# Optimization experiments

Measured on AMD Instinct MI355X. Metric: run time of the kernel, lower is better.

The kernel has to match this reference:

```python
import jax, jax.numpy as jnp
import numpy as np

B, T, D = 2, 2048, 1024
H, DK = 16, 64          # num_heads, head_dim (expand_v=1 -> d_v == d_k)
K = 4                    # short conv kernel size
EPS = 1e-5               # gated RMSNorm eps


def setup_inputs() -> dict:
    key = jax.random.key(0)
    ks = jax.random.split(key, 12)
    s = lambda d: d ** -0.5
    return {
        "x": jax.random.normal(ks[0], (B, T, D), jnp.float32),
        "Wq": jax.random.normal(ks[1], (D, H * DK), jnp.float32) * s(D),
        "Wk": jax.random.normal(ks[2], (D, H * DK), jnp.float32) * s(D),
        "Wv": jax.random.normal(ks[3], (D, H * DK), jnp.float32) * s(D),
        "Wa": jax.random.normal(ks[4], (D, H), jnp.float32) * s(D),
        "Wb": jax.random.normal(ks[5], (D, H), jnp.float32) * s(D),
        "Wg": jax.random.normal(ks[6], (D, H * DK), jnp.float32) * s(D),
        "Wo": jax.random.normal(ks[7], (H * DK, D), jnp.float32) * s(H * DK),
        "conv_q": jax.random.normal(ks[8], (H * DK, K), jnp.float32) * s(K),
        "conv_k": jax.random.normal(ks[9], (H * DK, K), jnp.float32) * s(K),
        "conv_v": jax.random.normal(ks[10], (H * DK, K), jnp.float32) * s(K),
        "A_log": jnp.log(jax.random.uniform(ks[11], (H,), jnp.float32, 1.0, 16.0)),
        "dt_bias": jnp.full((H,), 0.5, jnp.float32),
        "rms_w": jnp.ones((DK,), jnp.float32),
    }


def _short_conv(x, w):
    # causal depthwise conv1d (no bias) + silu; x: [B,T,C], w: [C,K]
    kk = w.shape[1]
    xp = jnp.pad(x, ((0, 0), (kk - 1, 0), (0, 0))).transpose(0, 2, 1)  # [B,C,T+K-1]
    y = jax.lax.conv_general_dilated(xp, w[:, None, :], (1,), 'VALID',
                                     feature_group_count=w.shape[0])
    return jax.nn.silu(y.transpose(0, 2, 1))


def _l2norm(x):
    return x * jax.lax.rsqrt(jnp.sum(x * x, -1, keepdims=True) + 1e-6)


def _gated_delta_rule(q, k, v, g, beta):
    # q,k,v: [B,T,H,Dk], g,beta: [B,T,H]; gated delta-rule linear attention
    scale = q.shape[-1] ** -0.5
    q = _l2norm(q) * scale
    k = _l2norm(k)
    qs, ks_, vs, gs, bs = (jnp.moveaxis(a, 1, 0) for a in (q, k, v, g, beta))
    h0 = jnp.zeros((q.shape[0], q.shape[2], q.shape[3], v.shape[3]), q.dtype)

    def step(h, t):
        qt, kt, vt, gt, bt = t
        h = h * jnp.exp(gt)[..., None, None]                      # decay state
        v_adj = (vt - jnp.einsum('bhk,bhkv->bhv', kt, h)) * bt[..., None]
        h = h + kt[..., None] * v_adj[:, :, None, :]              # rank-1 delta update
        ot = jnp.einsum('bhk,bhkv->bhv', qt, h)
        return h, ot

    _, o = jax.lax.scan(step, h0, (qs, ks_, vs, gs, bs))
    return jnp.moveaxis(o, 0, 1)  # [B,T,H,Dv]


def reference(x, Wq, Wk, Wv, Wa, Wb, Wg, Wo, conv_q, conv_k, conv_v, A_log, dt_bias, rms_w):
    q = _short_conv(x @ Wq, conv_q).reshape(B, T, H, DK)
    k = _short_conv(x @ Wk, conv_k).reshape(B, T, H, DK)
    v = _short_conv(x @ Wv, conv_v).reshape(B, T, H, DK)
    g = -jnp.exp(A_log) * jax.nn.softplus(x @ Wa + dt_bias)   # [B,T,H] log-decay
    beta = jax.nn.sigmoid(x @ Wb)                             # [B,T,H]
    o = _gated_delta_rule(q, k, v, g, beta)                   # [B,T,H,DK]
    gate = (x @ Wg).reshape(B, T, H, DK)
    o = o * jax.lax.rsqrt(jnp.mean(o * o, -1, keepdims=True) + EPS) * rms_w
    o = o * jax.nn.silu(gate)                                 # gated RMSNorm
    return o.reshape(B, T, H * DK) @ Wo
```

## Files before the change

### kernel.cpp

```cpp
#include <hip/hip_runtime.h>
#include <hip/hip_bf16.h>
#include <math.h>
#include <stdint.h>

#define BB 2
#define TT 2048
#define DD 1024
#define HH 16
#define DK 64
#define HD 1024
#define NC 32
#define CL 64
#define PAD 68
#define VS 16

typedef short bf16x8 __attribute__((ext_vector_type(8)));
typedef float f32x4 __attribute__((ext_vector_type(4)));
typedef unsigned short u16x8 __attribute__((ext_vector_type(8)));
typedef unsigned short u16x4 __attribute__((ext_vector_type(4)));

#define GAS __attribute__((address_space(1)))
#define LAS __attribute__((address_space(3)))

#define DOT4(a, b) ((a).x*(b).x + (a).y*(b).y + (a).z*(b).z + (a).w*(b).w)

#define OUT16(acc, kf, wv) \
    acc[0][0] += kf.x * wv.x; acc[0][1] += kf.x * wv.y; acc[0][2] += kf.x * wv.z; acc[0][3] += kf.x * wv.w; \
    acc[1][0] += kf.y * wv.x; acc[1][1] += kf.y * wv.y; acc[1][2] += kf.y * wv.z; acc[1][3] += kf.y * wv.w; \
    acc[2][0] += kf.z * wv.x; acc[2][1] += kf.z * wv.y; acc[2][2] += kf.z * wv.z; acc[2][3] += kf.z * wv.w; \
    acc[3][0] += kf.w * wv.x; acc[3][1] += kf.w * wv.y; acc[3][2] += kf.w * wv.z; acc[3][3] += kf.w * wv.w;

#define WSUB(c, hv) \
    acc[0][0] -= wa0.c * hv.x; acc[0][1] -= wa0.c * hv.y; acc[0][2] -= wa0.c * hv.z; acc[0][3] -= wa0.c * hv.w; \
    acc[1][0] -= wa1.c * hv.x; acc[1][1] -= wa1.c * hv.y; acc[1][2] -= wa1.c * hv.z; acc[1][3] -= wa1.c * hv.w; \
    acc[2][0] -= wa2.c * hv.x; acc[2][1] -= wa2.c * hv.y; acc[2][2] -= wa2.c * hv.z; acc[2][3] -= wa2.c * hv.w; \
    acc[3][0] -= wa3.c * hv.x; acc[3][1] -= wa3.c * hv.y; acc[3][2] -= wa3.c * hv.z; acc[3][3] -= wa3.c * hv.w;

#define ACC16(c, wv) \
    acc[0][0] += sa0.c * wv.x; acc[0][1] += sa0.c * wv.y; acc[0][2] += sa0.c * wv.z; acc[0][3] += sa0.c * wv.w; \
    acc[1][0] += sa1.c * wv.x; acc[1][1] += sa1.c * wv.y; acc[1][2] += sa1.c * wv.z; acc[1][3] += sa1.c * wv.w; \
    acc[2][0] += sa2.c * wv.x; acc[2][1] += sa2.c * wv.y; acc[2][2] += sa2.c * wv.z; acc[2][3] += sa2.c * wv.w; \
    acc[3][0] += sa3.c * wv.x; acc[3][1] += sa3.c * wv.y; acc[3][2] += sa3.c * wv.z; acc[3][3] += sa3.c * wv.w;

__device__ __forceinline__ float sigmoidf_(float x) { return 1.0f / (1.0f + expf(-x)); }
__device__ __forceinline__ float siluf_(float x) { return x * sigmoidf_(x); }

__device__ __forceinline__ unsigned short f2bf(float f) {
    unsigned int u = __builtin_bit_cast(unsigned int, f);
    u = (u + 0x7fffu + ((u >> 16) & 1u)) >> 16;
    return (unsigned short)u;
}

__global__ __launch_bounds__(256) void castx_k(const float* __restrict__ src,
                                               unsigned short* __restrict__ dst) {
    const size_t idx = (size_t)blockIdx.x * 256 + threadIdx.x;
    float4 a = *(const float4*)&src[idx * 8];
    float4 b = *(const float4*)&src[idx * 8 + 4];
    u16x8 o;
    o[0] = f2bf(a.x); o[1] = f2bf(a.y); o[2] = f2bf(a.z); o[3] = f2bf(a.w);
    o[4] = f2bf(b.x); o[5] = f2bf(b.y); o[6] = f2bf(b.z); o[7] = f2bf(b.w);
    *(u16x8*)&dst[idx * 8] = o;
}

__global__ __launch_bounds__(256) void castw_k(const float* __restrict__ W,
                                               unsigned short* __restrict__ Wt) {
    __shared__ float t_s[64][65];
    const int tid = threadIdx.x;
    const int rr = tid >> 4;
    const int cc = tid & 15;
    const int r0 = blockIdx.y * 64;
    const int c0 = blockIdx.x * 64;
#pragma unroll
    for (int i = 0; i < 4; ++i) {
        const int row = rr + i * 16;
        float4 v = *(const float4*)&W[(size_t)(r0 + row) * 1024 + c0 + cc * 4];
        t_s[row][cc * 4 + 0] = v.x;
        t_s[row][cc * 4 + 1] = v.y;
        t_s[row][cc * 4 + 2] = v.z;
        t_s[row][cc * 4 + 3] = v.w;
    }
    __syncthreads();
#pragma unroll
    for (int i = 0; i < 4; ++i) {
        const int nr = rr + i * 16;
        u16x4 o;
#pragma unroll
        for (int d = 0; d < 4; ++d) o[d] = f2bf(t_s[cc * 4 + d][nr]);
        *(u16x4*)&Wt[(size_t)(c0 + nr) * 1024 + r0 + cc * 4] = o;
    }
}

__global__ __launch_bounds__(256) void tw_k(const float* __restrict__ Wa,
                                            const float* __restrict__ Wb,
                                            float* __restrict__ Wt) {
    const int o = blockIdx.x;
    const int h = o & 15;
    const float* W = (o < 16) ? Wa : Wb;
    const int tid = threadIdx.x;
    float4 v;
    v.x = W[(size_t)(tid * 4 + 0) * HH + h];
    v.y = W[(size_t)(tid * 4 + 1) * HH + h];
    v.z = W[(size_t)(tid * 4 + 2) * HH + h];
    v.w = W[(size_t)(tid * 4 + 3) * HH + h];
    *(float4*)&Wt[(size_t)o * DD + tid * 4] = v;
}

__global__ __launch_bounds__(256) void gemm_bf16_k(const unsigned short* __restrict__ A,
                                                   const unsigned short* __restrict__ Bt,
                                                   float* __restrict__ C,
                                                   int M, int N, int Kd) {
    __shared__ unsigned short a_s[128 * 32];
    __shared__ unsigned short b_s[128 * 32];

    const int tid = threadIdx.x;
    const int wave = tid >> 6;
    const int lane = tid & 63;
    const int m0 = blockIdx.y * 128;
    const int n0 = blockIdx.x * 128;

    const int quad = lane >> 4;
    const int l16 = lane & 15;
    const int wr = wave >> 1;
    const int wc = wave & 1;

    const int srow = lane >> 2;
    const int sseg = lane & 3;

    f32x4 acc[4][4];
#pragma unroll
    for (int i = 0; i < 4; ++i)
#pragma unroll
        for (int j = 0; j < 4; ++j) acc[i][j] = (f32x4){0.f, 0.f, 0.f, 0.f};

    for (int k0 = 0; k0 < Kd; k0 += 32) {
        __syncthreads();
#pragma unroll
        for (int c = 0; c < 2; ++c) {
            const int region = wave * 2 + c;
            const int r0t = region * 16;
            const int ra = r0t + srow;
            const unsigned short* ga = A + (size_t)(m0 + ra) * Kd + k0 + sseg * 8;
            const unsigned short* gb = Bt + (size_t)(n0 + ra) * Kd + k0 + sseg * 8;
            __builtin_amdgcn_global_load_lds((const GAS unsigned int*)ga,
                                             (LAS unsigned int*)&a_s[r0t * 32], 16, 0, 0);
            __builtin_amdgcn_global_load_lds((const GAS unsigned int*)gb,
                                             (LAS unsigned int*)&b_s[r0t * 32], 16, 0, 0);
        }
        __syncthreads();

        bf16x8 af[4], bfr[4];
#pragma unroll
        for (int i = 0; i < 4; ++i)
            af[i] = *(const bf16x8*)&a_s[(wr * 64 + i * 16 + l16) * 32 + quad * 8];
#pragma unroll
        for (int j = 0; j < 4; ++j)
            bfr[j] = *(const bf16x8*)&b_s[(wc * 64 + j * 16 + l16) * 32 + quad * 8];
#pragma unroll
        for (int i = 0; i < 4; ++i)
#pragma unroll
            for (int j = 0; j < 4; ++j)
                acc[i][j] = __builtin_amdgcn_mfma_f32_16x16x32_bf16(af[i], bfr[j], acc[i][j], 0, 0, 0);
    }

#pragma unroll
    for (int i = 0; i < 4; ++i)
#pragma unroll
        for (int j = 0; j < 4; ++j) {
            const int col = n0 + wc * 64 + j * 16 + l16;
#pragma unroll
            for (int r = 0; r < 4; ++r) {
                const int row = m0 + wr * 64 + i * 16 + quad * 4 + r;
                C[(size_t)row * N + col] = acc[i][j][r];
            }
        }
}

__global__ __launch_bounds__(256) void gemm_qkvg_k(const unsigned short* __restrict__ A,
                                                   const unsigned short* __restrict__ Bt,
                                                   float* __restrict__ Oq,
                                                   float* __restrict__ Ok,
                                                   float* __restrict__ Ov,
                                                   float* __restrict__ Og) {
    __shared__ unsigned short a_s[128 * 32];
    __shared__ unsigned short b_s[128 * 32];

    const int tid = threadIdx.x;
    const int wave = tid >> 6;
    const int lane = tid & 63;
    const int m0 = blockIdx.y * 128;
    const int n0 = blockIdx.x * 128;

    const int quad = lane >> 4;
    const int l16 = lane & 15;
    const int wr = wave >> 1;
    const int wc = wave & 1;

    const int srow = lane >> 2;
    const int sseg = lane & 3;

    f32x4 acc[4][4];
#pragma unroll
    for (int i = 0; i < 4; ++i)
#pragma unroll
        for (int j = 0; j < 4; ++j) acc[i][j] = (f32x4){0.f, 0.f, 0.f, 0.f};

    for (int k0 = 0; k0 < DD; k0 += 32) {
        __syncthreads();
#pragma unroll
        for (int c = 0; c < 2; ++c) {
            const int region = wave * 2 + c;
            const int r0t = region * 16;
            const int ra = r0t + srow;
            const unsigned short* ga = A + (size_t)(m0 + ra) * DD + k0 + sseg * 8;
            const unsigned short* gb = Bt + (size_t)(n0 + ra) * DD + k0 + sseg * 8;
            __builtin_amdgcn_global_load_lds((const GAS unsigned int*)ga,
                                             (LAS unsigned int*)&a_s[r0t * 32], 16, 0, 0);
            __builtin_amdgcn_global_load_lds((const GAS unsigned int*)gb,
                                             (LAS unsigned int*)&b_s[r0t * 32], 16, 0, 0);
        }
        __syncthreads();

        bf16x8 af[4], bfr[4];
#pragma unroll
        for (int i = 0; i < 4; ++i)
            af[i] = *(const bf16x8*)&a_s[(wr * 64 + i * 16 + l16) * 32 + quad * 8];
#pragma unroll
        for (int j = 0; j < 4; ++j)
            bfr[j] = *(const bf16x8*)&b_s[(wc * 64 + j * 16 + l16) * 32 + quad * 8];
#pragma unroll
        for (int i = 0; i < 4; ++i)
#pragma unroll
            for (int j = 0; j < 4; ++j)
                acc[i][j] = __builtin_amdgcn_mfma_f32_16x16x32_bf16(af[i], bfr[j], acc[i][j], 0, 0, 0);
    }

    float* Cd = (n0 < 1024) ? Oq : (n0 < 2048) ? Ok : (n0 < 3072) ? Ov : Og;
    const int nl = n0 & 1023;
#pragma unroll
    for (int i = 0; i < 4; ++i)
#pragma unroll
        for (int j = 0; j < 4; ++j) {
            const int col = nl + wc * 64 + j * 16 + l16;
#pragma unroll
            for (int r = 0; r < 4; ++r) {
                const int row = m0 + wr * 64 + i * 16 + quad * 4 + r;
                Cd[(size_t)row * HD + col] = acc[i][j][r];
            }
        }
}

__global__ __launch_bounds__(256) void gbeta_k(const float* __restrict__ x,
                                               const float* __restrict__ Wt,
                                               const float* __restrict__ A_log,
                                               const float* __restrict__ dt_bias,
                                               float* __restrict__ g,
                                               float* __restrict__ beta) {
    __shared__ __align__(16) float xs[8][DD];
    const int r0 = blockIdx.x * 8;
    const int tid = threadIdx.x;

#pragma unroll
    for (int i = 0; i < 8; ++i) {
        const int f = tid + i * 256;
        const int r = f >> 8;
        const int col = (f & 255) * 4;
        *(float4*)&xs[r][col] = *(const float4*)&x[((size_t)r0 + r) * DD + col];
    }
    __syncthreads();

    const int out = tid >> 3;
    const int part = tid & 7;
    const int h = out & 15;
    const float* Wrow = Wt + (size_t)out * DD;

    float a0 = 0, a1 = 0, a2 = 0, a3 = 0, a4 = 0, a5 = 0, a6 = 0, a7 = 0;
#pragma unroll 4
    for (int i = 0; i < 32; ++i) {
        const int d = i * 32 + part * 4;
        const float4 wv = *(const float4*)&Wrow[d];
        float4 x0 = *(const float4*)&xs[0][d];
        float4 x1 = *(const float4*)&xs[1][d];
        float4 x2 = *(const float4*)&xs[2][d];
        float4 x3 = *(const float4*)&xs[3][d];
        float4 x4 = *(const float4*)&xs[4][d];
        float4 x5 = *(const float4*)&xs[5][d];
        float4 x6 = *(const float4*)&xs[6][d];
        float4 x7 = *(const float4*)&xs[7][d];
        a0 += DOT4(x0, wv); a1 += DOT4(x1, wv);
        a2 += DOT4(x2, wv); a3 += DOT4(x3, wv);
        a4 += DOT4(x4, wv); a5 += DOT4(x5, wv);
        a6 += DOT4(x6, wv); a7 += DOT4(x7, wv);
    }
#pragma unroll
    for (int s = 1; s <= 4; s <<= 1) {
        a0 += __shfl_xor(a0, s); a1 += __shfl_xor(a1, s);
        a2 += __shfl_xor(a2, s); a3 += __shfl_xor(a3, s);
        a4 += __shfl_xor(a4, s); a5 += __shfl_xor(a5, s);
        a6 += __shfl_xor(a6, s); a7 += __shfl_xor(a7, s);
    }

    if (part == 0) {
        float sv[8] = {a0, a1, a2, a3, a4, a5, a6, a7};
        if (out < 16) {
            const float ae = -expf(A_log[h]);
            const float db = dt_bias[h];
#pragma unroll
            for (int r = 0; r < 8; ++r) {
                float v = sv[r] + db;
                float sp = (v > 20.0f) ? v : log1pf(expf(v));
                g[((size_t)r0 + r) * HH + h] = ae * sp;
            }
        } else {
#pragma unroll
            for (int r = 0; r < 8; ++r)
                beta[((size_t)r0 + r) * HH + h] = sigmoidf_(sv[r]);
        }
    }
}

__global__ __launch_bounds__(64) void stage_k(const float* __restrict__ q_pre,
                                              const float* __restrict__ k_pre,
                                              const float* __restrict__ cq,
                                              const float* __restrict__ ck,
                                              const float* __restrict__ g,
                                              float* __restrict__ Qc,
                                              float* __restrict__ Kc,
                                              float* __restrict__ bcum) {
    const int blk = blockIdx.x;
    const int bh = blk >> 5;
    const int c = blk & 31;
    const int b = bh >> 4;
    const int h = bh & 15;
    const int lane = threadIdx.x;
    const int ch = h * DK + lane;

    const float4 wq4 = *(const float4*)&cq[ch * 4];
    const float4 wk4 = *(const float4*)&ck[ch * 4];

    float qw0 = 0, qw1 = 0, qw2 = 0, kw0 = 0, kw1 = 0, kw2 = 0;
    {
        const int t0 = c * CL;
        if (t0 - 3 >= 0) { size_t bi = ((size_t)b * TT + t0 - 3) * HD + ch; qw0 = q_pre[bi]; kw0 = k_pre[bi]; }
        if (t0 - 2 >= 0) { size_t bi = ((size_t)b * TT + t0 - 2) * HD + ch; qw1 = q_pre[bi]; kw1 = k_pre[bi]; }
        if (t0 - 1 >= 0) { size_t bi = ((size_t)b * TT + t0 - 1) * HD + ch; qw2 = q_pre[bi]; kw2 = k_pre[bi]; }
    }
    float* Qo = Qc + (size_t)blk * 4096;
    float* Ko = Kc + (size_t)blk * 4096;

    for (int tt = 0; tt < CL; ++tt) {
        const int t = c * CL + tt;
        const size_t bi = ((size_t)b * TT + t) * HD + ch;
        const float qc_ = q_pre[bi];
        const float kc_ = k_pre[bi];
        float qa = qw0 * wq4.x + qw1 * wq4.y + qw2 * wq4.z + qc_ * wq4.w;
        float ka = kw0 * wk4.x + kw1 * wk4.y + kw2 * wk4.z + kc_ * wk4.w;
        qw0 = qw1; qw1 = qw2; qw2 = qc_;
        kw0 = kw1; kw1 = kw2; kw2 = kc_;
        qa = siluf_(qa);
        ka = siluf_(ka);
        float qs2 = qa * qa, ks2 = ka * ka;
#pragma unroll
        for (int s = 32; s > 0; s >>= 1) {
            qs2 += __shfl_xor(qs2, s);
            ks2 += __shfl_xor(ks2, s);
        }
        Qo[tt * 64 + lane] = qa * rsqrtf(qs2 + 1e-6f) * 0.125f;
        Ko[tt * 64 + lane] = ka * rsqrtf(ks2 + 1e-6f);
    }

    float cum = g[((size_t)b * TT + c * CL + lane) * HH + h];
#pragma unroll
    for (int s = 1; s < 64; s <<= 1) {
        float u = __shfl_up(cum, s);
        if (lane >= s) cum += u;
    }
    bcum[(size_t)blk * 64 + lane] = cum;
}

__global__ __launch_bounds__(256) void prep_k(const float* __restrict__ Kc,
                                              const float* __restrict__ v_pre,
                                              const float* __restrict__ cv,
                                              const float* __restrict__ bcum,
                                              const float* __restrict__ bbuf,
                                              float* __restrict__ Wv,
                                              float* __restrict__ Wk) {
    __shared__ __align__(16) float k_s[CL * PAD];
    __shared__ __align__(16) float wv_s[CL * PAD];
    __shared__ __align__(16) float wk_s[CL * PAD];
    __shared__ __align__(16) float A_s[CL * PAD];
    __shared__ float T_s[4][16 * 17];
    __shared__ float b_s[CL], beta_s[CL], bk_s[CL];

    const int blk = blockIdx.x;
    const int bh = blk >> 5;
    const int c = blk & 31;
    const int b = bh >> 4;
    const int h = bh & 15;
    const int tid = threadIdx.x;

    if (tid < 64) {
        float bv = bcum[(size_t)blk * 64 + tid];
        float be = bbuf[((size_t)b * TT + c * CL + tid) * HH + h];
        b_s[tid] = bv;
        beta_s[tid] = be;
        bk_s[tid] = be * __expf(bv);
    }
    __syncthreads();

    {
        const float4* Kg = (const float4*)(Kc + (size_t)blk * 4096);
#pragma unroll
        for (int i = 0; i < 4; ++i) {
            int f = tid + i * 256;
            int t = f >> 4;
            int d = t * PAD + (f & 15) * 4;
            float4 kv = Kg[f];
            *(float4*)&k_s[d] = kv;
            float sk = bk_s[t];
            *(float4*)&wk_s[d] = make_float4(kv.x * sk, kv.y * sk, kv.z * sk, kv.w * sk);
        }
    }

    {
        const int lane = tid & 63;
        const int q4 = tid >> 6;
        const int ch = h * DK + lane;
        const float4 wv4 = *(const float4*)&cv[ch * 4];
        const int T0 = c * CL + q4 * 16;
        float w0 = 0, w1 = 0, w2 = 0;
        if (T0 - 3 >= 0) w0 = v_pre[((size_t)b * TT + T0 - 3) * HD + ch];
        if (T0 - 2 >= 0) w1 = v_pre[((size_t)b * TT + T0 - 2) * HD + ch];
        if (T0 - 1 >= 0) w2 = v_pre[((size_t)b * TT + T0 - 1) * HD + ch];
#pragma unroll 1
        for (int i = 0; i < 16; ++i) {
            const int t = T0 + i;
            const float vc_ = v_pre[((size_t)b * TT + t) * HD + ch];
            float va = w0 * wv4.x + w1 * wv4.y + w2 * wv4.z + vc_ * wv4.w;
            w0 = w1; w1 = w2; w2 = vc_;
            va = siluf_(va);
            wv_s[(q4 * 16 + i) * PAD + lane] = va * beta_s[q4 * 16 + i];
        }
    }
    __syncthreads();

    {
        const int t0 = (tid >> 4) * 4, s0 = (tid & 15) * 4;
        float acc[4][4] = {};
        for (int kk = 0; kk < 64; kk += 4) {
            float4 ta0 = *(const float4*)&k_s[(t0 + 0) * PAD + kk];
            float4 ta1 = *(const float4*)&k_s[(t0 + 1) * PAD + kk];
            float4 ta2 = *(const float4*)&k_s[(t0 + 2) * PAD + kk];
            float4 ta3 = *(const float4*)&k_s[(t0 + 3) * PAD + kk];
            float4 sb0 = *(const float4*)&k_s[(s0 + 0) * PAD + kk];
            float4 sb1 = *(const float4*)&k_s[(s0 + 1) * PAD + kk];
            float4 sb2 = *(const float4*)&k_s[(s0 + 2) * PAD + kk];
            float4 sb3 = *(const float4*)&k_s[(s0 + 3) * PAD + kk];
            acc[0][0] += DOT4(ta0, sb0); acc[0][1] += DOT4(ta0, sb1);
            acc[0][2] += DOT4(ta0, sb2); acc[0][3] += DOT4(ta0, sb3);
            acc[1][0] += DOT4(ta1, sb0); acc[1][1] += DOT4(ta1, sb1);
            acc[1][2] += DOT4(ta1, sb2); acc[1][3] += DOT4(ta1, sb3);
            acc[2][0] += DOT4(ta2, sb0); acc[2][1] += DOT4(ta2, sb1);
            acc[2][2] += DOT4(ta2, sb2); acc[2][3] += DOT4(ta2, sb3);
            acc[3][0] += DOT4(ta3, sb0); acc[3][1] += DOT4(ta3, sb1);
            acc[3][2] += DOT4(ta3, sb2); acc[3][3] += DOT4(ta3, sb3);
        }
        __syncthreads();
#pragma unroll
        for (int i = 0; i < 4; ++i)
#pragma unroll
            for (int j = 0; j < 4; ++j) {
                const int t = t0 + i, s = s0 + j;
                A_s[t * PAD + s] = (s < t) ? acc[i][j] * beta_s[t] * __expf(b_s[t] - b_s[s]) : 0.0f;
            }
    }
    __syncthreads();

    if (tid < 64) {
        const int d = tid >> 4;
        const int col = tid & 15;
        const int base = d * 16;
        float tcol[16];
#pragma unroll
        for (int s = 0; s < 16; ++s) tcol[s] = (s == col) ? 1.0f : 0.0f;
#pragma unroll
        for (int t = 1; t < 16; ++t) {
            float a = 0.0f;
#pragma unroll
            for (int s = 0; s < 16; ++s)
                if (s < t) a += A_s[(base + t) * PAD + base + s] * tcol[s];
            tcol[t] -= a;
        }
#pragma unroll
        for (int t = 0; t < 16; ++t) T_s[d][t * 17 + col] = tcol[t];
    }
    __syncthreads();

    {
        const int r = tid >> 4;
        const int cg = tid & 15;
        float* Wc = (cg < 8) ? wv_s : wk_s;
        const int cc = (cg & 7) * 8;

        for (int tb = 0; tb < 4; ++tb) {
            const int t = tb * 16 + r;
            if (tb > 0) {
                float4 lo = *(const float4*)&Wc[t * PAD + cc];
                float4 hi = *(const float4*)&Wc[t * PAD + cc + 4];
#pragma unroll 4
                for (int s = 0; s < tb * 16; ++s) {
                    const float a = A_s[t * PAD + s];
                    float4 wlo = *(const float4*)&Wc[s * PAD + cc];
                    float4 whi = *(const float4*)&Wc[s * PAD + cc + 4];
                    lo.x -= a * wlo.x; lo.y -= a * wlo.y; lo.z -= a * wlo.z; lo.w -= a * wlo.w;
                    hi.x -= a * whi.x; hi.y -= a * whi.y; hi.z -= a * whi.z; hi.w -= a * whi.w;
                }
                *(float4*)&Wc[t * PAD + cc] = lo;
                *(float4*)&Wc[t * PAD + cc + 4] = hi;
            }
            __syncthreads();
            float4 alo = make_float4(0, 0, 0, 0);
            float4 ahi = make_float4(0, 0, 0, 0);
#pragma unroll 4
            for (int s = 0; s < 16; ++s) {
                const float tv = T_s[tb][r * 17 + s];
                float4 wlo = *(const float4*)&Wc[(tb * 16 + s) * PAD + cc];
                float4 whi = *(const float4*)&Wc[(tb * 16 + s) * PAD + cc + 4];
                alo.x += tv * wlo.x; alo.y += tv * wlo.y; alo.z += tv * wlo.z; alo.w += tv * wlo.w;
                ahi.x += tv * whi.x; ahi.y += tv * whi.y; ahi.z += tv * whi.z; ahi.w += tv * whi.w;
            }
            __syncthreads();
            *(float4*)&Wc[t * PAD + cc] = alo;
            *(float4*)&Wc[t * PAD + cc + 4] = ahi;
            __syncthreads();
        }
    }

    float4* Wvg = (float4*)(Wv + (size_t)blk * 4096);
    float4* Wkg = (float4*)(Wk + (size_t)blk * 4096);
#pragma unroll
    for (int i = 0; i < 4; ++i) {
        int f = tid + i * 256;
        int d = (f >> 4) * PAD + (f & 15) * 4;
        Wvg[f] = *(float4*)&wv_s[d];
        Wkg[f] = *(float4*)&wk_s[d];
    }
}

__global__ __launch_bounds__(256) void ab_k(const float* __restrict__ Kc,
                                            const float* __restrict__ Wv,
                                            const float* __restrict__ Wk,
                                            const float* __restrict__ bcum,
                                            float* __restrict__ Ab,
                                            float* __restrict__ Bb) {
    __shared__ __align__(16) float kt_s[CL * PAD];
    __shared__ __align__(16) float wk_s[CL * PAD];
    __shared__ __align__(16) float wv_s[CL * PAD];
    __shared__ float e_s[CL];
    __shared__ float ebC_s;

    const int blk = blockIdx.x;
    const int tid = threadIdx.x;

    if (tid < 64) {
        float bC = bcum[(size_t)blk * 64 + 63];
        e_s[tid] = __expf(bC - bcum[(size_t)blk * 64 + tid]);
        if (tid == 63) ebC_s = __expf(bC);
    }
    __syncthreads();

    {
        const float4* Kg = (const float4*)(Kc + (size_t)blk * 4096);
        const float4* Wkg = (const float4*)(Wk + (size_t)blk * 4096);
        const float4* Wvg = (const float4*)(Wv + (size_t)blk * 4096);
#pragma unroll
        for (int i = 0; i < 4; ++i) {
            int f = tid + i * 256;
            int t = f >> 4;
            int d = t * PAD + (f & 15) * 4;
            float4 kv = Kg[f];
            float e = e_s[t];
            *(float4*)&kt_s[d] = make_float4(kv.x * e, kv.y * e, kv.z * e, kv.w * e);
            *(float4*)&wk_s[d] = Wkg[f];
            *(float4*)&wv_s[d] = Wvg[f];
        }
    }
    __syncthreads();

    const int k0 = (tid >> 4) * 4, m0 = (tid & 15) * 4;
    float aA[4][4] = {};
    float aB[4][4] = {};
    for (int ss = 0; ss < 64; ss += 4) {
        float4 kf0 = *(const float4*)&kt_s[(ss + 0) * PAD + k0];
        float4 kf1 = *(const float4*)&kt_s[(ss + 1) * PAD + k0];
        float4 kf2 = *(const float4*)&kt_s[(ss + 2) * PAD + k0];
        float4 kf3 = *(const float4*)&kt_s[(ss + 3) * PAD + k0];
        float4 wa0 = *(const float4*)&wk_s[(ss + 0) * PAD + m0];
        float4 wa1 = *(const float4*)&wk_s[(ss + 1) * PAD + m0];
        float4 wa2 = *(const float4*)&wk_s[(ss + 2) * PAD + m0];
        float4 wa3 = *(const float4*)&wk_s[(ss + 3) * PAD + m0];
        float4 wb0 = *(const float4*)&wv_s[(ss + 0) * PAD + m0];
        float4 wb1 = *(const float4*)&wv_s[(ss + 1) * PAD + m0];
        float4 wb2 = *(const float4*)&wv_s[(ss + 2) * PAD + m0];
        float4 wb3 = *(const float4*)&wv_s[(ss + 3) * PAD + m0];
        OUT16(aA, kf0, wa0); OUT16(aA, kf1, wa1); OUT16(aA, kf2, wa2); OUT16(aA, kf3, wa3);
        OUT16(aB, kf0, wb0); OUT16(aB, kf1, wb1); OUT16(aB, kf2, wb2); OUT16(aB, kf3, wb3);
    }

    const float ebC = ebC_s;
    float* Ag = Ab + (size_t)blk * 4096;
    float* Bg = Bb + (size_t)blk * 4096;
    const int p = tid & 15;
#pragma unroll
    for (int i = 0; i < 4; ++i) {
        const int kk = k0 + i;
        float4 av = make_float4(-aA[i][0], -aA[i][1], -aA[i][2], -aA[i][3]);
        if (kk - m0 == 0) av.x += ebC;
        if (kk - m0 == 1) av.y += ebC;
        if (kk - m0 == 2) av.z += ebC;
        if (kk - m0 == 3) av.w += ebC;
        *(float4*)&Ag[p * 256 + kk * 4] = av;
        *(float4*)&Bg[kk * 64 + m0] = make_float4(aB[i][0], aB[i][1], aB[i][2], aB[i][3]);
    }
}

__global__ __launch_bounds__(64) void hrec_k(const float* __restrict__ Ab,
                                             const float* __restrict__ Bb,
                                             float* __restrict__ Hst) {
    const int blk = blockIdx.x;
    const int bh = blk & 31;
    const int vs = blk >> 5;
    const int k = threadIdx.x;

    __shared__ __align__(16) float A_lds[2][4096];
    __shared__ __align__(16) float h_s[4][64];

#pragma unroll
    for (int j = 0; j < 4; ++j) h_s[j][k] = 0.0f;
    float h0 = 0, h1 = 0, h2 = 0, h3 = 0;

    const float* Abase = Ab + (size_t)bh * NC * 4096;
    const float* Bbase = Bb + (size_t)bh * NC * 4096 + k * 64 + vs * 4;
    float* Hbase = Hst + (size_t)bh * NC * 4096 + k * 64 + vs * 4;

    const LAS float* rd_cur = (const LAS float*)&A_lds[0][0] + k * 4;
    const LAS float* rd_nxt = (const LAS float*)&A_lds[1][0] + k * 4;

#pragma unroll
    for (int i = 0; i < 16; ++i)
        __builtin_amdgcn_global_load_lds((const GAS unsigned int*)(Abase + i * 256 + k * 4),
                                         (LAS unsigned int*)&A_lds[0][i * 256], 16, 0, 0);
    float4 bn = *(const float4*)&Bbase[0];

#pragma unroll 1
    for (int c = 0; c < NC; ++c) {
        float4 b0 = bn;

        *(float4*)&Hbase[(size_t)c * 4096] = make_float4(h0, h1, h2, h3);

        if (c + 1 < NC) {
            const float* An = Abase + (size_t)(c + 1) * 4096;
#pragma unroll
            for (int i = 0; i < 16; ++i)
                __builtin_amdgcn_global_load_lds((const GAS unsigned int*)(An + i * 256 + k * 4),
                                                 (LAS unsigned int*)(rd_nxt - (size_t)k * 4 + i * 256),
                                                 16, 0, 0);
            bn = *(const float4*)&Bbase[(size_t)(c + 1) * 4096];
            asm volatile("s_waitcnt vmcnt(18)" ::: "memory");
        } else {
            asm volatile("s_waitcnt vmcnt(1)" ::: "memory");
        }
        __builtin_amdgcn_sched_barrier(0);

        f32x4 ar0, ar1, ar2, ar3, ar4, ar5, ar6, ar7;
        f32x4 ar8, ar9, ar10, ar11, ar12, ar13, ar14, ar15;
#define ARD(DST, OFF) asm volatile("ds_read_b128 %0, %1 offset:" OFF \
                                   : "=v"(DST) : "v"(rd_cur))
        ARD(ar0, "0");      ARD(ar1, "1024");   ARD(ar2, "2048");   ARD(ar3, "3072");
        ARD(ar4, "4096");   ARD(ar5, "5120");   ARD(ar6, "6144");   ARD(ar7, "7168");
        ARD(ar8, "8192");   ARD(ar9, "9216");   ARD(ar10, "10240"); ARD(ar11, "11264");
        ARD(ar12, "12288"); ARD(ar13, "13312"); ARD(ar14, "14336"); ARD(ar15, "15360");
#undef ARD
        asm volatile("s_waitcnt lgkmcnt(0)" ::: "memory");
        __builtin_amdgcn_sched_barrier(0);

        float a0 = b0.x, a1 = b0.y, a2 = b0.z, a3 = b0.w;
#define HFMA(AR, M4) { \
        const float4 hv0 = *(const float4*)&h_s[0][(M4) * 4]; \
        const float4 hv1 = *(const float4*)&h_s[1][(M4) * 4]; \
        const float4 hv2 = *(const float4*)&h_s[2][(M4) * 4]; \
        const float4 hv3 = *(const float4*)&h_s[3][(M4) * 4]; \
        a0 += AR[0] * hv0.x + AR[1] * hv0.y + AR[2] * hv0.z + AR[3] * hv0.w; \
        a1 += AR[0] * hv1.x + AR[1] * hv1.y + AR[2] * hv1.z + AR[3] * hv1.w; \
        a2 += AR[0] * hv2.x + AR[1] * hv2.y + AR[2] * hv2.z + AR[3] * hv2.w; \
        a3 += AR[0] * hv3.x + AR[1] * hv3.y + AR[2] * hv3.z + AR[3] * hv3.w; }
        HFMA(ar0, 0)   HFMA(ar1, 1)   HFMA(ar2, 2)   HFMA(ar3, 3)
        HFMA(ar4, 4)   HFMA(ar5, 5)   HFMA(ar6, 6)   HFMA(ar7, 7)
        HFMA(ar8, 8)   HFMA(ar9, 9)   HFMA(ar10, 10) HFMA(ar11, 11)
        HFMA(ar12, 12) HFMA(ar13, 13) HFMA(ar14, 14) HFMA(ar15, 15)
#undef HFMA

        h0 = a0; h1 = a1; h2 = a2; h3 = a3;
        h_s[0][k] = h0; h_s[1][k] = h1; h_s[2][k] = h2; h_s[3][k] = h3;

        const LAS float* t = rd_cur; rd_cur = rd_nxt; rd_nxt = t;
    }
}

__global__ __launch_bounds__(256) void wfix_k(const float* __restrict__ Wk,
                                              const float* __restrict__ Hst,
                                              float* __restrict__ Wio) {
    __shared__ __align__(16) float wk_s[CL * PAD];
    __shared__ __align__(16) float h_s[CL * PAD];

    const int blk = blockIdx.x;
    const int tid = threadIdx.x;

    {
        const float4* Wkg = (const float4*)(Wk + (size_t)blk * 4096);
        const float4* Hg = (const float4*)(Hst + (size_t)blk * 4096);
#pragma unroll
        for (int i = 0; i < 4; ++i) {
            int f = tid + i * 256;
            int d = (f >> 4) * PAD + (f & 15) * 4;
            *(float4*)&wk_s[d] = Wkg[f];
            *(float4*)&h_s[d] = Hg[f];
        }
    }
    __syncthreads();

    const int t0 = (tid >> 4) * 4, v0 = (tid & 15) * 4;
    float* Wg = Wio + (size_t)blk * 4096;

    float acc[4][4];
#pragma unroll
    for (int i = 0; i < 4; ++i) {
        float4 wv = *(const float4*)&Wg[(t0 + i) * 64 + v0];
        acc[i][0] = wv.x; acc[i][1] = wv.y; acc[i][2] = wv.z; acc[i][3] = wv.w;
    }
    for (int kk = 0; kk < 64; kk += 4) {
        float4 wa0 = *(const float4*)&wk_s[(t0 + 0) * PAD + kk];
        float4 wa1 = *(const float4*)&wk_s[(t0 + 1) * PAD + kk];
        float4 wa2 = *(const float4*)&wk_s[(t0 + 2) * PAD + kk];
        float4 wa3 = *(const float4*)&wk_s[(t0 + 3) * PAD + kk];
        float4 hb0 = *(const float4*)&h_s[(kk + 0) * PAD + v0];
        float4 hb1 = *(const float4*)&h_s[(kk + 1) * PAD + v0];
        float4 hb2 = *(const float4*)&h_s[(kk + 2) * PAD + v0];
        float4 hb3 = *(const float4*)&h_s[(kk + 3) * PAD + v0];
        WSUB(x, hb0); WSUB(y, hb1); WSUB(z, hb2); WSUB(w, hb3);
    }
#pragma unroll
    for (int i = 0; i < 4; ++i)
        *(float4*)&Wg[(t0 + i) * 64 + v0] =
            make_float4(acc[i][0], acc[i][1], acc[i][2], acc[i][3]);
}

__global__ __launch_bounds__(256) void out_k(const float* __restrict__ Qc,
                                             const float* __restrict__ Kc,
                                             const float* __restrict__ Wb_,
                                             const float* __restrict__ Hst,
                                             const float* __restrict__ bcum,
                                             float* __restrict__ o_scan) {
    __shared__ __align__(16) float q_s[CL * PAD];
    __shared__ __align__(16) float s_s[CL * PAD];
    __shared__ __align__(16) float h_s[CL * PAD];
    __shared__ __align__(16) float w_s[CL * PAD];
    __shared__ float b_s[64];

    const int blk = blockIdx.x;
    const int bh = blk >> 5;
    const int c = blk & 31;
    const int b = bh >> 4;
    const int h = bh & 15;
    const int tid = threadIdx.x;

    if (tid < 64) b_s[tid] = bcum[(size_t)blk * 64 + tid];
    {
        const float4* Qg = (const float4*)(Qc + (size_t)blk * 4096);
        const float4* Kg = (const float4*)(Kc + (size_t)blk * 4096);
        const float4* Hg = (const float4*)(Hst + (size_t)blk * 4096);
        const float4* Wg = (const float4*)(Wb_ + (size_t)blk * 4096);
#pragma unroll
        for (int i = 0; i < 4; ++i) {
            int f = tid + i * 256;
            int d = (f >> 4) * PAD + (f & 15) * 4;
            *(float4*)&q_s[d] = Qg[f];
            *(float4*)&s_s[d] = Kg[f];
            *(float4*)&h_s[d] = Hg[f];
            *(float4*)&w_s[d] = Wg[f];
        }
    }
    __syncthreads();

    {
        const int t0 = (tid >> 4) * 4, s0 = (tid & 15) * 4;
        float acc[4][4] = {};
        for (int kk = 0; kk < 64; kk += 4) {
            float4 ta0 = *(const float4*)&q_s[(t0 + 0) * PAD + kk];
            float4 ta1 = *(const float4*)&q_s[(t0 + 1) * PAD + kk];
            float4 ta2 = *(const float4*)&q_s[(t0 + 2) * PAD + kk];
            float4 ta3 = *(const float4*)&q_s[(t0 + 3) * PAD + kk];
            float4 sb0 = *(const float4*)&s_s[(s0 + 0) * PAD + kk];
            float4 sb1 = *(const float4*)&s_s[(s0 + 1) * PAD + kk];
            float4 sb2 = *(const float4*)&s_s[(s0 + 2) * PAD + kk];
            float4 sb3 = *(const float4*)&s_s[(s0 + 3) * PAD + kk];
            acc[0][0] += DOT4(ta0, sb0); acc[0][1] += DOT4(ta0, sb1);
            acc[0][2] += DOT4(ta0, sb2); acc[0][3] += DOT4(ta0, sb3);
            acc[1][0] += DOT4(ta1, sb0); acc[1][1] += DOT4(ta1, sb1);
            acc[1][2] += DOT4(ta1, sb2); acc[1][3] += DOT4(ta1, sb3);
            acc[2][0] += DOT4(ta2, sb0); acc[2][1] += DOT4(ta2, sb1);
            acc[2][2] += DOT4(ta2, sb2); acc[2][3] += DOT4(ta2, sb3);
            acc[3][0] += DOT4(ta3, sb0); acc[3][1] += DOT4(ta3, sb1);
            acc[3][2] += DOT4(ta3, sb2); acc[3][3] += DOT4(ta3, sb3);
        }
        __syncthreads();
#pragma unroll
        for (int i = 0; i < 4; ++i)
#pragma unroll
            for (int j = 0; j < 4; ++j) {
                const int t = t0 + i, s = s0 + j;
                s_s[t * PAD + s] = (s <= t) ? acc[i][j] * __expf(b_s[t] - b_s[s]) : 0.0f;
            }
    }
#pragma unroll
    for (int i = 0; i < 16; ++i) {
        const int e = tid + i * 256;
        const int t = e >> 6;
        q_s[t * PAD + (e & 63)] *= __expf(b_s[t]);
    }
    __syncthreads();

    {
        const int t0 = (tid >> 4) * 4, v0 = (tid & 15) * 4;
        float acc[4][4] = {};
        for (int ss = 0; ss < 64; ss += 4) {
            float4 sa0 = *(const float4*)&s_s[(t0 + 0) * PAD + ss];
            float4 sa1 = *(const float4*)&s_s[(t0 + 1) * PAD + ss];
            float4 sa2 = *(const float4*)&s_s[(t0 + 2) * PAD + ss];
            float4 sa3 = *(const float4*)&s_s[(t0 + 3) * PAD + ss];
            float4 wb0 = *(const float4*)&w_s[(ss + 0) * PAD + v0];
            float4 wb1 = *(const float4*)&w_s[(ss + 1) * PAD + v0];
            float4 wb2 = *(const float4*)&w_s[(ss + 2) * PAD + v0];
            float4 wb3 = *(const float4*)&w_s[(ss + 3) * PAD + v0];
            ACC16(x, wb0); ACC16(y, wb1); ACC16(z, wb2); ACC16(w, wb3);
        }
        for (int kk = 0; kk < 64; kk += 4) {
            float4 sa0 = *(const float4*)&q_s[(t0 + 0) * PAD + kk];
            float4 sa1 = *(const float4*)&q_s[(t0 + 1) * PAD + kk];
            float4 sa2 = *(const float4*)&q_s[(t0 + 2) * PAD + kk];
            float4 sa3 = *(const float4*)&q_s[(t0 + 3) * PAD + kk];
            float4 wb0 = *(const float4*)&h_s[(kk + 0) * PAD + v0];
            float4 wb1 = *(const float4*)&h_s[(kk + 1) * PAD + v0];
            float4 wb2 = *(const float4*)&h_s[(kk + 2) * PAD + v0];
            float4 wb3 = *(const float4*)&h_s[(kk + 3) * PAD + v0];
            ACC16(x, wb0); ACC16(y, wb1); ACC16(z, wb2); ACC16(w, wb3);
        }
#pragma unroll
        for (int i = 0; i < 4; ++i) {
            const int t = c * CL + t0 + i;
            *(float4*)&o_scan[(((size_t)b * TT + t) * HH + h) * DK + v0] =
                make_float4(acc[i][0], acc[i][1], acc[i][2], acc[i][3]);
        }
    }
}

__global__ __launch_bounds__(256) void gnorm_k(const float* __restrict__ o_scan,
                                               const float* __restrict__ gate,
                                               const float* __restrict__ rms_w,
                                               unsigned short* __restrict__ o2) {
    const int tid = threadIdx.x;
    const int grp = tid >> 6;
    const int lane = tid & 63;
    const int bth = blockIdx.x * 4 + grp;
    const int h = bth & 15;
    const int row = bth >> 4;

    float ov = o_scan[(size_t)bth * DK + lane];
    float s = ov * ov;
#pragma unroll
    for (int sh = 32; sh > 0; sh >>= 1) s += __shfl_xor(s, sh);
    float r = rsqrtf(s * (1.0f / 64.0f) + 1e-5f);

    float gt = gate[(size_t)row * HD + h * DK + lane];
    o2[(size_t)row * HD + h * DK + lane] = f2bf(ov * r * rms_w[lane] * siluf_(gt));
}

extern "C" void kernel_launch(void* const* d_in, const int* in_sizes, int n_in,
                              void* d_out, int out_size, void* d_ws, size_t ws_size,
                              hipStream_t stream) {
    (void)in_sizes; (void)n_in; (void)out_size; (void)ws_size;

    const float* x       = (const float*)d_in[0];
    const float* Wq      = (const float*)d_in[1];
    const float* Wk_     = (const float*)d_in[2];
    const float* Wv_     = (const float*)d_in[3];
    const float* Wa      = (const float*)d_in[4];
    const float* Wb      = (const float*)d_in[5];
    const float* Wg      = (const float*)d_in[6];
    const float* Wo      = (const float*)d_in[7];
    const float* conv_q  = (const float*)d_in[8];
    const float* conv_k  = (const float*)d_in[9];
    const float* conv_v  = (const float*)d_in[10];
    const float* A_log   = (const float*)d_in[11];
    const float* dt_bias = (const float*)d_in[12];
    const float* rms_w   = (const float*)d_in[13];
    float* out = (float*)d_out;

    float* ws = (float*)d_ws;
    const size_t NTOK = (size_t)BB * TT;
    const size_t BIG = NTOK * HD;

    float* q_pre = ws + 0 * BIG;
    float* k_pre = ws + 1 * BIG;
    float* v_pre = ws + 2 * BIG;
    float* gatep = ws + 3 * BIG;
    float* Qc    = ws + 4 * BIG;
    float* Kc    = ws + 5 * BIG;
    float* gbuf  = ws + 6 * BIG;
    float* bbuf  = gbuf + NTOK * HH;
    float* bcumb = bbuf + NTOK * HH;

    unsigned short* xb  = (unsigned short*)(bcumb + NTOK * HH);
    unsigned short* wqt = xb + (size_t)NTOK * DD;
    unsigned short* wkt = wqt + (size_t)DD * HD;
    unsigned short* wvt = wkt + (size_t)DD * HD;
    unsigned short* wgt = wvt + (size_t)DD * HD;
    unsigned short* wot = wgt + (size_t)DD * HD;

    float* Bbuf = (float*)(wot + (size_t)DD * HD);
    float* HstB = Bbuf + BIG;
    float* Wabt = HstB + BIG;

    float* Wvb    = q_pre;
    float* Wkb    = k_pre;
    float* Abuf   = v_pre;
    float* o_scan = v_pre;
    unsigned short* o2b = (unsigned short*)Qc;

    castx_k<<<(int)(NTOK * DD / (256 * 8)), 256, 0, stream>>>(x, xb);
    dim3 tg(16, 16);
    castw_k<<<tg, 256, 0, stream>>>(Wq, wqt);
    castw_k<<<tg, 256, 0, stream>>>(Wk_, wkt);
    castw_k<<<tg, 256, 0, stream>>>(Wv_, wvt);
    castw_k<<<tg, 256, 0, stream>>>(Wg, wgt);
    castw_k<<<tg, 256, 0, stream>>>(Wo, wot);
    tw_k<<<32, 256, 0, stream>>>(Wa, Wb, Wabt);

    gemm_qkvg_k<<<dim3(32, 32), 256, 0, stream>>>(xb, wqt, q_pre, k_pre, v_pre, gatep);

    gbeta_k<<<(int)(NTOK / 8), 256, 0, stream>>>(x, Wabt, A_log, dt_bias, gbuf, bbuf);

    stage_k<<<BB * HH * NC, 64, 0, stream>>>(q_pre, k_pre, conv_q, conv_k, gbuf,
                                             Qc, Kc, bcumb);

    prep_k<<<BB * HH * NC, 256, 0, stream>>>(Kc, v_pre, conv_v, bcumb, bbuf, Wvb, Wkb);

    ab_k<<<BB * HH * NC, 256, 0, stream>>>(Kc, Wvb, Wkb, bcumb, Abuf, Bbuf);
    hrec_k<<<BB * HH * VS, 64, 0, stream>>>(Abuf, Bbuf, HstB);
    wfix_k<<<BB * HH * NC, 256, 0, stream>>>(Wkb, HstB, Wvb);

    out_k<<<BB * HH * NC, 256, 0, stream>>>(Qc, Kc, Wvb, HstB, bcumb, o_scan);

    gnorm_k<<<(int)(NTOK * HH / 4), 256, 0, stream>>>(o_scan, gatep, rms_w, o2b);

    gemm_bf16_k<<<dim3(HD / 128, NTOK / 128), 256, 0, stream>>>(o2b, wot, out,
                                                                (int)NTOK, HD, DD);
}
```

Measured before the change: 470.4 us.

## Rewrite QKVG projection GEMM with 256x256 tiles, double-buffered swizzled LDS

After: 446.1 us. -5.2%, faster.

```diff
diff --git a/kernel.cpp b/kernel.cpp
--- a/kernel.cpp
+++ b/kernel.cpp
@@ -175,77 +175,147 @@
         }
 }
 
-__global__ __launch_bounds__(256) void gemm_qkvg_k(const unsigned short* __restrict__ A,
-                                                   const unsigned short* __restrict__ Bt,
-                                                   float* __restrict__ Oq,
-                                                   float* __restrict__ Ok,
-                                                   float* __restrict__ Ov,
-                                                   float* __restrict__ Og) {
-    __shared__ unsigned short a_s[128 * 32];
-    __shared__ unsigned short b_s[128 * 32];
+#define DSRQ(D, P, OFF) asm volatile("ds_read_b128 %0, %1 offset:" OFF \
+                                     : "=v"(D) : "v"(P))
+
+__global__ __launch_bounds__(512, 2) void gemm_qkvg_k(const unsigned short* __restrict__ A,
+                                                      const unsigned short* __restrict__ Bt,
+                                                      float* __restrict__ Oq,
+                                                      float* __restrict__ Ok,
+                                                      float* __restrict__ Ov,
+                                                      float* __restrict__ Og) {
+    __shared__ __align__(16) unsigned char lds_all[131072];
 
     const int tid = threadIdx.x;
-    const int wave = tid >> 6;
+    const int w = tid >> 6;
     const int lane = tid & 63;
-    const int m0 = blockIdx.y * 128;
-    const int n0 = blockIdx.x * 128;
-
+    const int l16 = lane & 15;
     const int quad = lane >> 4;
-    const int l16 = lane & 15;
-    const int wr = wave >> 1;
-    const int wc = wave & 1;
-
-    const int srow = lane >> 2;
-    const int sseg = lane & 3;
-
-    f32x4 acc[4][4];
-#pragma unroll
-    for (int i = 0; i < 4; ++i)
+    const int wr = w >> 2;
+    const int wc = w & 3;
+
+    const int bid = blockIdx.x;
+    const int wg = (bid & 7) * 32 + (bid >> 3);
+    const int m0 = (wg >> 4) * 256;
+    const int n0 = (wg & 15) * 256;
+
+    const int lr = lane >> 3;
+    const int ls = lane & 7;
+    const int sslot = ls ^ lr;
+    const unsigned short* srcA = A + (size_t)(m0 + lr) * DD + sslot * 8 + (size_t)w * 8 * DD;
+    const unsigned short* srcB = Bt + (size_t)(n0 + lr) * DD + sslot * 8 + (size_t)w * 8 * DD;
+
+    const LAS unsigned char* LB = (const LAS unsigned char*)&lds_all[0];
+
+    const unsigned int xq = (unsigned int)((quad ^ (l16 & 7)) << 4);
+    const unsigned int uA0 = (unsigned int)((wr * 128 + l16) * 128) + xq;
+    const unsigned int uB0 = 65536u + (unsigned int)((wc * 64 + l16) * 128) + xq;
+
+    f32x4 acc[8][4];
+#pragma unroll
+    for (int i = 0; i < 8; ++i)
 #pragma unroll
         for (int j = 0; j < 4; ++j) acc[i][j] = (f32x4){0.f, 0.f, 0.f, 0.f};
 
-    for (int k0 = 0; k0 < DD; k0 += 32) {
-        __syncthreads();
-#pragma unroll
-        for (int c = 0; c < 2; ++c) {
-            const int region = wave * 2 + c;
-            const int r0t = region * 16;
-            const int ra = r0t + srow;
-            const unsigned short* ga = A + (size_t)(m0 + ra) * DD + k0 + sseg * 8;
-            const unsigned short* gb = Bt + (size_t)(n0 + ra) * DD + k0 + sseg * 8;
-            __builtin_amdgcn_global_load_lds((const GAS unsigned int*)ga,
-                                             (LAS unsigned int*)&a_s[r0t * 32], 16, 0, 0);
-            __builtin_amdgcn_global_load_lds((const GAS unsigned int*)gb,
-                                             (LAS unsigned int*)&b_s[r0t * 32], 16, 0, 0);
-        }
-        __syncthreads();
-
-        bf16x8 af[4], bfr[4];
-#pragma unroll
-        for (int i = 0; i < 4; ++i)
-            af[i] = *(const bf16x8*)&a_s[(wr * 64 + i * 16 + l16) * 32 + quad * 8];
-#pragma unroll
-        for (int j = 0; j < 4; ++j)
-            bfr[j] = *(const bf16x8*)&b_s[(wc * 64 + j * 16 + l16) * 32 + quad * 8];
-#pragma unroll
-        for (int i = 0; i < 4; ++i)
+#define STG1Q(T, IA) \
+    __builtin_amdgcn_global_load_lds( \
+        (const GAS unsigned int*)(srcA + (size_t)(IA) * 65536 + (size_t)(T) * 64), \
+        (LAS unsigned int*)(LB + (((unsigned)((T) & 1)) << 15) + ((IA) * 8 + w) * 1024), 16, 0, 0); \
+    __builtin_amdgcn_global_load_lds( \
+        (const GAS unsigned int*)(srcB + (size_t)(IA) * 65536 + (size_t)(T) * 64), \
+        (LAS unsigned int*)(LB + 65536u + (((unsigned)((T) & 1)) << 15) + ((IA) * 8 + w) * 1024), 16, 0, 0);
+#define STGQ(T) { STG1Q(T, 0) STG1Q(T, 1) STG1Q(T, 2) STG1Q(T, 3) }
+
+    STGQ(0);
+
+    bf16x8 aG0[4], aG1[4], b0[4], b1[4];
+
+#pragma unroll 1
+    for (int t = 0; t < 16; ++t) {
+        if (t + 1 < 16) {
+            STGQ(t + 1);
+            asm volatile("s_waitcnt vmcnt(8)" ::: "memory");
+        } else {
+            asm volatile("s_waitcnt vmcnt(0)" ::: "memory");
+        }
+        __builtin_amdgcn_s_barrier();
+
+        const unsigned int boff = ((unsigned)(t & 1)) << 15;
+        const LAS unsigned char* pA0 = LB + (uA0 + boff);
+        const LAS unsigned char* pA1 = LB + ((uA0 ^ 64u) + boff);
+        const LAS unsigned char* pB0 = LB + (uB0 + boff);
+        const LAS unsigned char* pB1 = LB + ((uB0 ^ 64u) + boff);
+
+        DSRQ(b0[0], pB0, "0");    DSRQ(b0[1], pB0, "2048");
+        DSRQ(b0[2], pB0, "4096"); DSRQ(b0[3], pB0, "6144");
+        DSRQ(aG0[0], pA0, "0");    DSRQ(aG0[1], pA0, "2048");
+        DSRQ(aG0[2], pA0, "4096"); DSRQ(aG0[3], pA0, "6144");
+        DSRQ(aG1[0], pA0, "8192");  DSRQ(aG1[1], pA0, "10240");
+        DSRQ(aG1[2], pA0, "12288"); DSRQ(aG1[3], pA0, "14336");
+        DSRQ(b1[0], pB1, "0");    DSRQ(b1[1], pB1, "2048");
+        DSRQ(b1[2], pB1, "4096"); DSRQ(b1[3], pB1, "6144");
+
+        asm volatile("s_waitcnt lgkmcnt(8)" ::: "memory");
+        __builtin_amdgcn_sched_barrier(0);
+        __builtin_amdgcn_s_setprio(1);
+#pragma unroll
+        for (int ia = 0; ia < 4; ++ia)
 #pragma unroll
             for (int j = 0; j < 4; ++j)
-                acc[i][j] = __builtin_amdgcn_mfma_f32_16x16x32_bf16(af[i], bfr[j], acc[i][j], 0, 0, 0);
-    }
+                acc[ia][j] = __builtin_amdgcn_mfma_f32_16x16x32_bf16(aG0[ia], b0[j], acc[ia][j], 0, 0, 0);
+        __builtin_amdgcn_s_setprio(0);
+
+        DSRQ(aG0[0], pA1, "0");    DSRQ(aG0[1], pA1, "2048");
+        DSRQ(aG0[2], pA1, "4096"); DSRQ(aG0[3], pA1, "6144");
+        asm volatile("s_waitcnt lgkmcnt(4)" ::: "memory");
+        __builtin_amdgcn_sched_barrier(0);
+        __builtin_amdgcn_s_setprio(1);
+#pragma unroll
+        for (int ia = 0; ia < 4; ++ia)
+#pragma unroll
+            for (int j = 0; j < 4; ++j)
+                acc[4 + ia][j] = __builtin_amdgcn_mfma_f32_16x16x32_bf16(aG1[ia], b0[j], acc[4 + ia][j], 0, 0, 0);
+        __builtin_amdgcn_s_setprio(0);
+
+        DSRQ(aG1[0], pA1, "8192");  DSRQ(aG1[1], pA1, "10240");
+        DSRQ(aG1[2], pA1, "12288"); DSRQ(aG1[3], pA1, "14336");
+        asm volatile("s_waitcnt lgkmcnt(4)" ::: "memory");
+        __builtin_amdgcn_sched_barrier(0);
+        __builtin_amdgcn_s_setprio(1);
+#pragma unroll
+        for (int ia = 0; ia < 4; ++ia)
+#pragma unroll
+            for (int j = 0; j < 4; ++j)
+                acc[ia][j] = __builtin_amdgcn_mfma_f32_16x16x32_bf16(aG0[ia], b1[j], acc[ia][j], 0, 0, 0);
+        __builtin_amdgcn_s_setprio(0);
+
+        asm volatile("s_waitcnt lgkmcnt(0)" ::: "memory");
+        __builtin_amdgcn_sched_barrier(0);
+        __builtin_amdgcn_s_setprio(1);
+#pragma unroll
+        for (int ia = 0; ia < 4; ++ia)
+#pragma unroll
+            for (int j = 0; j < 4; ++j)
+                acc[4 + ia][j] = __builtin_amdgcn_mfma_f32_16x16x32_bf16(aG1[ia], b1[j], acc[4 + ia][j], 0, 0, 0);
+        __builtin_amdgcn_s_setprio(0);
+
+        __builtin_amdgcn_s_barrier();
+    }
+#undef STGQ
+#undef STG1Q
 
     float* Cd = (n0 < 1024) ? Oq : (n0 < 2048) ? Ok : (n0 < 3072) ? Ov : Og;
     const int nl = n0 & 1023;
-#pragma unroll
-    for (int i = 0; i < 4; ++i)
+    const int rbase = m0 + wr * 128 + quad * 4;
+    const int cbase = nl + wc * 64 + l16;
+#pragma unroll
+    for (int ia = 0; ia < 8; ++ia)
 #pragma unroll
         for (int j = 0; j < 4; ++j) {
-            const int col = nl + wc * 64 + j * 16 + l16;
-#pragma unroll
-            for (int r = 0; r < 4; ++r) {
-                const int row = m0 + wr * 64 + i * 16 + quad * 4 + r;
-                Cd[(size_t)row * HD + col] = acc[i][j][r];
-            }
+            const int col = cbase + j * 16;
+#pragma unroll
+            for (int r = 0; r < 4; ++r)
+                Cd[(size_t)(rbase + ia * 16 + r) * HD + col] = acc[ia][j][r];
         }
 }
 
@@ -945,7 +1015,7 @@
     castw_k<<<tg, 256, 0, stream>>>(Wo, wot);
     tw_k<<<32, 256, 0, stream>>>(Wa, Wb, Wabt);
 
-    gemm_qkvg_k<<<dim3(32, 32), 256, 0, stream>>>(xb, wqt, q_pre, k_pre, v_pre, gatep);
+    gemm_qkvg_k<<<256, 512, 0, stream>>>(xb, wqt, q_pre, k_pre, v_pre, gatep);
 
     gbeta_k<<<(int)(NTOK / 8), 256, 0, stream>>>(x, Wabt, A_log, dt_bias, gbuf, bbuf);
 
```
